# Kernel tuning notes

Measured on AMD Instinct MI355X. Metric: run time of the kernel, lower is better.

Reference implementation:

```python
import jax, jax.numpy as jnp
import numpy as np

B, S, D = 2, 2048, 2048
VOCAB = 32000
CUTOFFS = [1000, 2000, 5000, VOCAB]  # torch appends vocab_size
N_CLUSTERS = 3
HEAD_SIZE = CUTOFFS[0] + N_CLUSTERS  # 1003
LN_EPS = 1e-5
INIT = 0.02


def setup_inputs() -> dict:
    key = jax.random.key(0)
    ks = jax.random.split(key, 10)
    inp = {
        "x": jax.random.normal(ks[0], (B, S, D), dtype=jnp.float32),
        "targets": jax.random.randint(ks[1], (B, S), 0, VOCAB, dtype=jnp.int32),
        "gamma": jnp.ones((D,), jnp.float32),
        "beta": jnp.zeros((D,), jnp.float32),
        "head_w": jax.random.normal(ks[2], (HEAD_SIZE, D), jnp.float32) * INIT,
    }
    # tail clusters: hsz = D // 4**i, osz = cutoffs[i] - cutoffs[i-1]
    for i in range(1, 4):
        hsz = D // (4 ** i)
        osz = CUTOFFS[i] - CUTOFFS[i - 1]
        inp[f"t{i}_w1"] = jax.random.normal(ks[2 + 2 * i], (hsz, D), jnp.float32) * INIT
        inp[f"t{i}_w2"] = jax.random.normal(ks[3 + 2 * i], (osz, hsz), jnp.float32) * INIT
    return inp


def reference(x, targets, gamma, beta, head_w, t1_w1, t1_w2, t2_w1, t2_w2, t3_w1, t3_w2):
    # LayerNorm over last dim
    mu = jnp.mean(x, axis=-1, keepdims=True)
    var = jnp.mean(jnp.square(x - mu), axis=-1, keepdims=True)
    xn = (x - mu) * jax.lax.rsqrt(var + LN_EPS) * gamma + beta

    # shift: predict token t+1 from hidden t
    h = xn[:, :-1, :].reshape(-1, x.shape[-1])      # [N, D]
    lbl = targets[:, 1:].reshape(-1)                # [N]
    n = h.shape[0]
    rows = jnp.arange(n)

    # head: shortlist (first cutoff) + one logit per tail cluster
    head_lp = jax.nn.log_softmax(h @ head_w.T, axis=-1)  # [N, 1003]
    out = head_lp[rows, jnp.clip(lbl, 0, CUTOFFS[0] - 1)]

    tails = [(t1_w1, t1_w2), (t2_w1, t2_w2), (t3_w1, t3_w2)]
    for i, (w1, w2) in enumerate(tails):
        low, high = CUTOFFS[i], CUTOFFS[i + 1]
        tail_lp = jax.nn.log_softmax((h @ w1.T) @ w2.T, axis=-1)  # [N, osz]
        rel = jnp.clip(lbl - low, 0, high - low - 1)
        lp = head_lp[:, CUTOFFS[0] + i] + tail_lp[rows, rel]
        out = jnp.where((lbl >= low) & (lbl < high), lp, out)

    return -jnp.mean(out)  # NLL loss, matches .loss of AdaptiveLogSoftmaxWithLoss
```

## Files before the change

kernel.cpp:

```cpp
#include <hip/hip_runtime.h>
#include <hip/hip_bf16.h>
#include <math.h>

#define BB 2
#define SS 2048
#define DD 2048
#define NR (BB*(SS-1))
#define NRP 4096
#define MT_LD 768
#define MT_P2 512
#define MT_P3 640

#define L2E 1.4426950408889634f
#define LN2F 0.6931471805599453f
#define LSE_SHIFT 4.0f
#define LSE_NC (-LSE_SHIFT * L2E)
#define WSCALE 16.0f
#define WINV   0.0625f

typedef short  bh8   __attribute__((ext_vector_type(8)));
typedef float  f32x4 __attribute__((ext_vector_type(4)));
typedef long   l64x2 __attribute__((ext_vector_type(2)));

__device__ inline float bfl(unsigned short b) { return __uint_as_float(((unsigned)b) << 16); }
__device__ inline float expsh(float v) { return __builtin_amdgcn_exp2f(fmaf(v, L2E, LSE_NC)); }

__device__ inline float block_sum256(float v) {
    __shared__ float tmp[4];
    #pragma unroll
    for (int o = 32; o > 0; o >>= 1) v += __shfl_down(v, o, 64);
    int lane = threadIdx.x & 63, w = threadIdx.x >> 6;
    if (lane == 0) tmp[w] = v;
    __syncthreads();
    float r = tmp[0] + tmp[1] + tmp[2] + tmp[3];
    __syncthreads();
    return r;
}

__device__ inline unsigned pack_fp8x4(float a, float b, float c, float d) {
    unsigned r = 0;
    r = __builtin_amdgcn_cvt_pk_fp8_f32(a, b, r, false);
    r = __builtin_amdgcn_cvt_pk_fp8_f32(c, d, r, true);
    return r;
}

struct CastSegs {
    const float* src[7];
    void* dst[7];
    int n_src[7];
    int n_tot[7];
    int b0[7];
    int isfp8[7];
    float scl[7];
};
struct AParams {
    const float* x; const float* gamma; const float* beta;
    unsigned char* h8;
    CastSegs sg; int castBlocks;
    const int* targets;
    int *relH, *rel1, *rel2, *rel3;
    float *S0, *S1, *S2, *out;
};

__global__ __launch_bounds__(256) void stageA(AParams p) {
    int blk = blockIdx.x, tid = threadIdx.x;
    if (blk < NRP) {
        int n = blk;
        unsigned char* hr = p.h8 + (size_t)n * DD;
        if (n >= NR) { *(uint2*)(hr + tid * 8) = make_uint2(0,0); return; }
        int b = n / (SS - 1), t = n % (SS - 1);
        const float4* xr = (const float4*)(p.x + (size_t)(b * SS + t) * DD);
        float4 a = xr[tid * 2];
        float4 c = xr[tid * 2 + 1];
        float sum = a.x + a.y + a.z + a.w + c.x + c.y + c.z + c.w;
        sum = block_sum256(sum);
        float mu = sum * (1.0f / DD);
        float d[8] = {a.x-mu, a.y-mu, a.z-mu, a.w-mu, c.x-mu, c.y-mu, c.z-mu, c.w-mu};
        float sq = 0.f;
        #pragma unroll
        for (int i = 0; i < 8; ++i) sq += d[i] * d[i];
        sq = block_sum256(sq);
        float rstd = rsqrtf(sq * (1.0f / DD) + 1e-5f);
        const float4* g4 = (const float4*)p.gamma;
        const float4* be4 = (const float4*)p.beta;
        float4 g1 = g4[tid*2], g2 = g4[tid*2+1];
        float4 b1 = be4[tid*2], b2 = be4[tid*2+1];
        float gg[8] = {g1.x,g1.y,g1.z,g1.w,g2.x,g2.y,g2.z,g2.w};
        float bb[8] = {b1.x,b1.y,b1.z,b1.w,b2.x,b2.y,b2.z,b2.w};
        float o[8];
        #pragma unroll
        for (int i = 0; i < 8; ++i) o[i] = d[i] * rstd * gg[i] + bb[i];
        uint2 pk;
        pk.x = pack_fp8x4(o[0], o[1], o[2], o[3]);
        pk.y = pack_fp8x4(o[4], o[5], o[6], o[7]);
        *(uint2*)(hr + tid * 8) = pk;
        return;
    }
    blk -= NRP;
    if (blk < p.castBlocks) {
        int k = 0;
        #pragma unroll
        for (int i = 1; i < 7; ++i) if (blk >= p.sg.b0[i]) k = i;
        int i4 = (blk - p.sg.b0[k]) * 1024 + tid * 4;
        if (i4 >= p.sg.n_tot[k]) return;
        float4 v = make_float4(0.f,0.f,0.f,0.f);
        if (i4 < p.sg.n_src[k]) v = *(const float4*)(p.sg.src[k] + i4);
        if (p.sg.isfp8[k]) {
            unsigned pk = pack_fp8x4(v.x * WSCALE, v.y * WSCALE, v.z * WSCALE, v.w * WSCALE);
            *(unsigned*)((unsigned char*)p.sg.dst[k] + i4) = pk;
        } else {
            float sc = p.sg.scl[k];
            __align__(8) __hip_bfloat16 o[4] = {
                __float2bfloat16(v.x * sc), __float2bfloat16(v.y * sc),
                __float2bfloat16(v.z * sc), __float2bfloat16(v.w * sc)};
            *(uint2*)((__hip_bfloat16*)p.sg.dst[k] + i4) = *(uint2*)o;
        }
        return;
    }
    blk -= p.castBlocks;
    int n = blk * 256 + tid;
    if (n >= NRP) return;
    int lbl = -1;
    if (n < NR) {
        int b = n / (SS - 1), t = n % (SS - 1);
        lbl = p.targets[b * SS + t + 1];
    }
    bool v = n < NR;
    p.relH[n] = v ? (lbl < 1000 ? lbl : 999) : -1;
    int r1 = lbl - 1000;  p.rel1[n] = v ? (r1 < 0 ? 0 : (r1 > 999   ? 999   : r1)) : -1;
    int r2 = lbl - 2000;  p.rel2[n] = v ? (r2 < 0 ? 0 : (r2 > 2999  ? 2999  : r2)) : -1;
    int r3 = lbl - 5000;  p.rel3[n] = v ? (r3 < 0 ? 0 : (r3 > 26999 ? 26999 : r3)) : -1;
    p.S0[n] = 0.f; p.S1[n] = 0.f; p.S2[n] = 0.f;
    if (n == 0) p.out[0] = 0.f;
}

__global__ __launch_bounds__(256) void megaF(
        const unsigned char* __restrict__ A,
        const unsigned char* __restrict__ W,
        __hip_bfloat16* __restrict__ megaT,
        const int* __restrict__ relH,
        float* __restrict__ S0, float* __restrict__ aux) {
    __shared__ __align__(16) unsigned char smF[2][12288];
    int tid = threadIdx.x, wv = tid >> 6, lane = tid & 63;
    int row0 = blockIdx.y * 64, col0 = blockIdx.x * 128;
    int wrow = (wv >> 1) * 32, wcol = (wv & 1) * 64;
    f32x4 acc[2][4];
    #pragma unroll
    for (int i = 0; i < 2; ++i)
        #pragma unroll
        for (int j = 0; j < 4; ++j) acc[i][j] = (f32x4){0.f,0.f,0.f,0.f};
    int sr = lane >> 2;
    int kp = (((lane & 3) ^ (sr & 3)) * 16);
    int mrow = lane & 15;
    int qx = (((lane >> 4) ^ (lane & 3)) * 16);

    auto stage = [&](int buf, int k0) {
        {
            int r = wv * 16 + sr;
            const void* ga = A + (size_t)(row0 + r) * DD + k0 + kp;
            void* la = (char*)&smF[buf][0] + wv * 1024 + lane * 16;
            __builtin_amdgcn_global_load_lds(
                (const __attribute__((address_space(1))) void*)ga,
                (__attribute__((address_space(3))) void*)la, 16, 0, 0);
        }
        #pragma unroll
        for (int i = 0; i < 2; ++i) {
            int chunk = wv * 2 + i;
            int r = chunk * 16 + sr;
            const void* gw = W + (size_t)(col0 + r) * DD + k0 + kp;
            void* lw = (char*)&smF[buf][4096] + chunk * 1024 + lane * 16;
            __builtin_amdgcn_global_load_lds(
                (const __attribute__((address_space(1))) void*)gw,
                (__attribute__((address_space(3))) void*)lw, 16, 0, 0);
        }
    };

    stage(0, 0);
    asm volatile("s_waitcnt vmcnt(0)" ::: "memory");
    __builtin_amdgcn_s_barrier();
    __builtin_amdgcn_sched_barrier(0);
    int cur = 0;
    for (int k0 = 0; k0 < DD; k0 += 64) {
        if (k0 + 64 < DD) stage(cur ^ 1, k0 + 64);
        const unsigned char* As = &smF[cur][0];
        const unsigned char* Ws = &smF[cur][4096];
        l64x2 af[2], bfr[4];
        #pragma unroll
        for (int t = 0; t < 2; ++t)
            af[t]  = *(const l64x2*)(As + (wrow + t*16 + mrow) * 64 + qx);
        #pragma unroll
        for (int t = 0; t < 4; ++t)
            bfr[t] = *(const l64x2*)(Ws + (wcol + t*16 + mrow) * 64 + qx);
        #pragma unroll
        for (int s = 0; s < 2; ++s)
            #pragma unroll
            for (int i = 0; i < 2; ++i)
                #pragma unroll
                for (int j = 0; j < 4; ++j)
                    acc[i][j] = __builtin_amdgcn_mfma_f32_16x16x32_fp8_fp8(
                        af[i][s], bfr[j][s], acc[i][j], 0, 0, 0);
        asm volatile("s_waitcnt vmcnt(0) lgkmcnt(0)" ::: "memory");
        __builtin_amdgcn_s_barrier();
        __builtin_amdgcn_sched_barrier(0);
        cur ^= 1;
    }
    int ccol = lane & 15, g = lane >> 4;
    if (blockIdx.x < 8) {
        int grs[2][4], rh[2][4];
        float ps[2][4];
        #pragma unroll
        for (int i = 0; i < 2; ++i)
            #pragma unroll
            for (int r = 0; r < 4; ++r) {
                grs[i][r] = row0 + wrow + i*16 + g*4 + r;
                rh[i][r] = relH[grs[i][r]];
                ps[i][r] = 0.f;
            }
        #pragma unroll
        for (int i = 0; i < 2; ++i)
            #pragma unroll
            for (int j = 0; j < 4; ++j) {
                int gc = col0 + wcol + j*16 + ccol;
                bool inr = gc < 1003;
                #pragma unroll
                for (int r = 0; r < 4; ++r) {
                    float v = acc[i][j][r] * WINV;
                    if (gc == rh[i][r]) aux[grs[i][r]*8 + 0] = v;
                    if (gc >= 1000 && gc < 1003) aux[grs[i][r]*8 + 2 + (gc - 1000)] = v;
                    ps[i][r] += inr ? expsh(v) : 0.f;
                }
            }
        #pragma unroll
        for (int off = 1; off < 16; off <<= 1)
            #pragma unroll
            for (int i = 0; i < 2; ++i)
                #pragma unroll
                for (int r = 0; r < 4; ++r) ps[i][r] += __shfl_xor(ps[i][r], off, 64);
        if (ccol == 0)
            #pragma unroll
            for (int i = 0; i < 2; ++i)
                #pragma unroll
                for (int r = 0; r < 4; ++r) atomicAdd(&S0[grs[i][r]], ps[i][r]);
    } else {
        int cb = col0 - 1024 + wcol;
        #pragma unroll
        for (int i = 0; i < 2; ++i) {
            size_t gr0 = row0 + wrow + i*16 + g*4;
            #pragma unroll
            for (int j = 0; j < 4; ++j) {
                size_t gc = cb + j*16 + ccol;
                #pragma unroll
                for (int r = 0; r < 4; ++r)
                    megaT[(gr0 + r) * MT_LD + gc] = __float2bfloat16(acc[i][j][r] * WINV);
            }
        }
    }
}

__device__ void tail_gemm(const __hip_bfloat16* A, int lda,
        const __hip_bfloat16* W, int K, int bx, int by, int validCols,
        const int* rel, float* S, float* tgt, char* sm) {
    __hip_bfloat16* As = (__hip_bfloat16*)sm;
    __hip_bfloat16* Ws = (__hip_bfloat16*)(sm + 4096);
    int tid = threadIdx.x, wv = tid >> 6, lane = tid & 63;
    int row0 = by * 64, col0 = bx * 128;
    int wrow = (wv >> 1) * 32, wcol = (wv & 1) * 64;
    f32x4 acc[2][4];
    #pragma unroll
    for (int i = 0; i < 2; ++i)
        #pragma unroll
        for (int j = 0; j < 4; ++j) acc[i][j] = (f32x4){0.f,0.f,0.f,0.f};
    int sr = lane >> 2;
    int sk = (((lane & 3) ^ (sr & 3)) * 8);
    int mrow = lane & 15;
    int qx = (((lane >> 4) ^ (lane & 3)) * 16);

    for (int k0 = 0; k0 < K; k0 += 32) {
        __syncthreads();
        #pragma unroll
        for (int i = 0; i < 3; ++i) {
            int c = wv * 3 + i;
            const __hip_bfloat16* gsrc;
            char* ldst;
            if (c < 4) {
                gsrc = A + (size_t)(row0 + c * 16 + sr) * lda + k0 + sk;
                ldst = (char*)As + c * 1024 + lane * 16;
            } else {
                int cw = c - 4;
                gsrc = W + (size_t)(col0 + cw * 16 + sr) * K + k0 + sk;
                ldst = (char*)Ws + cw * 1024 + lane * 16;
            }
            __builtin_amdgcn_global_load_lds(
                (const __attribute__((address_space(1))) void*)gsrc,
                (__attribute__((address_space(3))) void*)ldst, 16, 0, 0);
        }
        __syncthreads();
        bh8 af[2], bfr[4];
        #pragma unroll
        for (int t = 0; t < 2; ++t)
            af[t] = *(const bh8*)((const char*)As + (wrow + t*16 + mrow) * 64 + qx);
        #pragma unroll
        for (int t = 0; t < 4; ++t)
            bfr[t] = *(const bh8*)((const char*)Ws + (wcol + t*16 + mrow) * 64 + qx);
        #pragma unroll
        for (int i = 0; i < 2; ++i)
            #pragma unroll
            for (int j = 0; j < 4; ++j)
                acc[i][j] = __builtin_amdgcn_mfma_f32_16x16x32_bf16(af[i], bfr[j], acc[i][j], 0, 0, 0);
    }
    int ccol = lane & 15, g = lane >> 4;
    int grs[2][4], rh[2][4];
    float p[2][4];
    #pragma unroll
    for (int i = 0; i < 2; ++i)
        #pragma unroll
        for (int r = 0; r < 4; ++r) {
            grs[i][r] = row0 + wrow + i*16 + g*4 + r;
            rh[i][r] = rel[grs[i][r]];
            p[i][r] = 0.f;
        }
    #pragma unroll
    for (int i = 0; i < 2; ++i)
        #pragma unroll
        for (int j = 0; j < 4; ++j) {
            int gc = col0 + wcol + j*16 + ccol;
            bool inr = gc < validCols;
            #pragma unroll
            for (int r = 0; r < 4; ++r) {
                float v = acc[i][j][r];
                if (gc == rh[i][r]) tgt[grs[i][r]] = v;
                p[i][r] += inr ? expsh(v) : 0.f;
            }
        }
    #pragma unroll
    for (int off = 1; off < 16; off <<= 1)
        #pragma unroll
        for (int i = 0; i < 2; ++i)
            #pragma unroll
            for (int r = 0; r < 4; ++r) p[i][r] += __shfl_xor(p[i][r], off, 64);
    if (ccol == 0)
        #pragma unroll
        for (int i = 0; i < 2; ++i)
            #pragma unroll
            for (int r = 0; r < 4; ++r) atomicAdd(&S[grs[i][r]], p[i][r]);
}

#define T3_TILES 1688
#define T3_SPLIT 32
#define T3_TPC   53
__device__ void t3_partial_body(const __hip_bfloat16* megaT,
        const __hip_bfloat16* w2b, float* pS, int idx, int tid, float* red ) {
    int rg = idx >> 5, cs = idx & 31;
    int wv = tid >> 6, lane = tid & 63;
    int q = lane >> 4, cm = lane & 15;
    int row0 = rg * 64;
    bh8 af[4];
    #pragma unroll
    for (int h = 0; h < 4; ++h)
        af[h] = *(const bh8*)(megaT + (size_t)(row0 + h*16 + cm) * MT_LD + MT_P3 + q * 8);
    int tile0 = cs * T3_TPC;
    int tile1 = tile0 + T3_TPC; if (tile1 > T3_TILES) tile1 = T3_TILES;
    float s[4][4];
    #pragma unroll
    for (int h = 0; h < 4; ++h)
        #pragma unroll
        for (int r = 0; r < 4; ++r) s[h][r] = 0.f;
    int ot = tile0 + wv;
    auto baddr = [&](int t) {
        int tc = t < tile1 ? t : tile1 - 1;
        return (const bh8*)(w2b + (size_t)(tc * 16 + cm) * 32 + q * 8);
    };
    bh8 p0 = *baddr(ot), p1 = *baddr(ot + 4), p2 = *baddr(ot + 8), p3 = *baddr(ot + 12);
    for (; ot < tile1; ot += 4) {
        bh8 bcur = p0;
        p0 = p1; p1 = p2; p2 = p3;
        int otn = ot + 16;
        if (otn < tile1)
            p3 = *(const bh8*)(w2b + (size_t)(otn * 16 + cm) * 32 + q * 8);
        f32x4 c[4];
        #pragma unroll
        for (int h = 0; h < 4; ++h)
            c[h] = __builtin_amdgcn_mfma_f32_16x16x32_bf16(af[h], bcur, (f32x4){0,0,0,0}, 0, 0, 0);
        #pragma unroll
        for (int h = 0; h < 4; ++h)
            #pragma unroll
            for (int r = 0; r < 4; ++r) s[h][r] += __builtin_amdgcn_exp2f(c[h][r]);
    }
    #pragma unroll
    for (int off = 1; off < 16; off <<= 1)
        #pragma unroll
        for (int h = 0; h < 4; ++h)
            #pragma unroll
            for (int r = 0; r < 4; ++r) s[h][r] += __shfl_xor(s[h][r], off, 64);
    if (cm == 0)
        #pragma unroll
        for (int h = 0; h < 4; ++h)
            #pragma unroll
            for (int r = 0; r < 4; ++r)
                red[wv * 64 + h*16 + q*4 + r] = s[h][r];
    __syncthreads();
    if (tid < 64)
        pS[(size_t)(row0 + tid) * T3_SPLIT + cs] =
            red[tid] + red[64 + tid] + red[128 + tid] + red[192 + tid];
}

__device__ void t3_gather_body(const __hip_bfloat16* megaT, const __hip_bfloat16* w2b,
        const int* rel3, float* tt2, int idx, int tid) {
    int n = idx * 256 + tid;
    if (n >= NR) return;
    int rc = rel3[n];
    const unsigned short* pa = (const unsigned short*)(megaT + (size_t)n * MT_LD + MT_P3);
    const unsigned short* pw = (const unsigned short*)(w2b + (size_t)rc * 32);
    float acc = 0.f;
    #pragma unroll
    for (int k = 0; k < 32; ++k) acc += bfl(pa[k]) * bfl(pw[k]);
    tt2[n] = acc;
}

#define NT3 (64 * T3_SPLIT)
#define NT1 512
#define NT2 1536
__global__ __launch_bounds__(256) void fatC(const __hip_bfloat16* __restrict__ megaT,
        const __hip_bfloat16* __restrict__ t1w2b, const __hip_bfloat16* __restrict__ t2w2b,
        const __hip_bfloat16* __restrict__ w2b3,
        const int* __restrict__ rel1, const int* __restrict__ rel2, const int* __restrict__ rel3,
        float* __restrict__ S1, float* __restrict__ S2, float* __restrict__ pS3,
        float* __restrict__ tt0, float* __restrict__ tt1, float* __restrict__ tt2) {
    __shared__ __align__(16) char sm[12288];
    int idx = blockIdx.x, tid = threadIdx.x;
    if (idx < NT3) { t3_partial_body(megaT, w2b3, pS3, idx, tid, (float*)sm); return; }
    idx -= NT3;
    if (idx < NT1) { tail_gemm(megaT, MT_LD, t1w2b, 512, idx % 8, idx / 8, 1000, rel1, S1, tt0, sm); return; }
    idx -= NT1;
    if (idx < NT2) { tail_gemm(megaT + MT_P2, MT_LD, t2w2b, 128, idx % 24, idx / 24, 3000, rel2, S2, tt1, sm); return; }
    idx -= NT2;
    t3_gather_body(megaT, w2b3, rel3, tt2, idx, tid);
}

__global__ __launch_bounds__(256) void final_kernel(const float* __restrict__ aux,
        const int* __restrict__ targets,
        const float* __restrict__ S0, const float* __restrict__ S1, const float* __restrict__ S2,
        const float* __restrict__ pS3,
        const float* __restrict__ tt0, const float* __restrict__ tt1, const float* __restrict__ tt2,
        float* __restrict__ out) {
    int n = blockIdx.x * 256 + threadIdx.x;
    float local = 0.f;
    if (n < NR) {
        int b = n / (SS - 1), t = n % (SS - 1);
        int lbl = targets[b * SS + t + 1];
        float lse = logf(S0[n]) + LSE_SHIFT;
        float o;
        if (lbl < 1000)      o = aux[n*8 + 0] - lse;
        else if (lbl < 2000) o = (aux[n*8 + 2] - lse) + (tt0[n] - (logf(S1[n]) + LSE_SHIFT));
        else if (lbl < 5000) o = (aux[n*8 + 3] - lse) + (tt1[n] - (logf(S2[n]) + LSE_SHIFT));
        else {
            float S3 = 0.f;
            const float4* p4 = (const float4*)(pS3 + (size_t)n * T3_SPLIT);
            #pragma unroll
            for (int c = 0; c < T3_SPLIT/4; ++c) {
                float4 v = p4[c];
                S3 += v.x + v.y + v.z + v.w;
            }
            S3 -= 8.0f;
            o = (aux[n*8 + 4] - lse) + (tt2[n] * LN2F - logf(S3));
        }
        local = o;
    }
    local = block_sum256(local);
    if (threadIdx.x == 0) atomicAdd(out, -local / (float)NR);
}

extern "C" void kernel_launch(void* const* d_in, const int* in_sizes, int n_in,
                              void* d_out, int out_size, void* d_ws, size_t ws_size,
                              hipStream_t stream) {
    const float* x      = (const float*)d_in[0];
    const int*   targets= (const int*)d_in[1];
    const float* gamma  = (const float*)d_in[2];
    const float* beta   = (const float*)d_in[3];
    const float* head_w = (const float*)d_in[4];
    const float* t1_w1  = (const float*)d_in[5];
    const float* t1_w2  = (const float*)d_in[6];
    const float* t2_w1  = (const float*)d_in[7];
    const float* t2_w2  = (const float*)d_in[8];
    const float* t3_w1  = (const float*)d_in[9];
    const float* t3_w2  = (const float*)d_in[10];
    (void)in_sizes; (void)n_in; (void)out_size; (void)ws_size;

    char* base = (char*)d_ws;
    size_t off = 0;
    auto ab = [&](size_t nbytes) { char* p = base + off; off += (nbytes + 15) & ~(size_t)15; return p; };
    unsigned char* h8     = (unsigned char*)ab((size_t)NRP * DD);
    unsigned char* w1cat8 = (unsigned char*)ab((size_t)1792 * DD);
    __hip_bfloat16* megaT = (__hip_bfloat16*)ab((size_t)NRP * MT_LD * 2);
    __hip_bfloat16* t1w2b = (__hip_bfloat16*)ab((size_t)1024 * 512 * 2);
    __hip_bfloat16* t2w2b = (__hip_bfloat16*)ab((size_t)3072 * 128 * 2);
    __hip_bfloat16* w2b3  = (__hip_bfloat16*)ab((size_t)27008 * 32 * 2);
    float* aux = (float*)ab((size_t)NRP * 8 * 4);
    float* pS3 = (float*)ab((size_t)NRP * T3_SPLIT * 4);
    float* S0  = (float*)ab(NRP * 4);
    float* S1  = (float*)ab(NRP * 4);
    float* S2  = (float*)ab(NRP * 4);
    int* relH  = (int*)ab(NRP * 4);
    int* rel1  = (int*)ab(NRP * 4);
    int* rel2  = (int*)ab(NRP * 4);
    int* rel3  = (int*)ab(NRP * 4);
    float* tt0 = (float*)ab(NRP * 4);
    float* tt1 = (float*)ab(NRP * 4);
    float* tt2 = (float*)ab(NRP * 4);

    AParams p;
    p.x = x; p.gamma = gamma; p.beta = beta; p.h8 = h8;
    p.targets = targets;
    p.relH = relH; p.rel1 = rel1; p.rel2 = rel2; p.rel3 = rel3;
    p.S0 = S0; p.S1 = S1; p.S2 = S2; p.out = (float*)d_out;
    const float* srcs[7] = {head_w, t1_w1, t2_w1, t3_w1, t1_w2, t2_w2, t3_w2};
    void* dsts[7] = {w1cat8, w1cat8 + (size_t)1024*2048, w1cat8 + (size_t)1536*2048,
                     w1cat8 + (size_t)1664*2048, t1w2b, t2w2b, w2b3};
    int nsrc[7] = {1003*2048, 512*2048, 128*2048, 32*2048, 1000*512, 3000*128, 27000*32};
    int ntot[7] = {1024*2048, 512*2048, 128*2048, 128*2048, 1024*512, 3072*128, 27008*32};
    int isf8[7] = {1, 1, 1, 1, 0, 0, 0};
    float scls[7] = {1.f, 1.f, 1.f, 1.f, 1.0f, 1.0f, L2E};
    int blk = 0;
    for (int i = 0; i < 7; ++i) {
        p.sg.src[i] = srcs[i]; p.sg.dst[i] = dsts[i];
        p.sg.n_src[i] = nsrc[i]; p.sg.n_tot[i] = ntot[i];
        p.sg.isfp8[i] = isf8[i];
        p.sg.scl[i] = scls[i];
        p.sg.b0[i] = blk;
        blk += (ntot[i] + 1023) / 1024;
    }
    p.castBlocks = blk;

    stageA<<<NRP + blk + 16, 256, 0, stream>>>(p);
    megaF<<<dim3(14, 64), 256, 0, stream>>>(h8, w1cat8, megaT, relH, S0, aux);
    fatC<<<NT3 + NT1 + NT2 + 16, 256, 0, stream>>>(megaT, t1w2b, t2w2b, w2b3,
            rel1, rel2, rel3, S1, S2, pS3, tt0, tt1, tt2);
    final_kernel<<<16, 256, 0, stream>>>(aux, targets, S0, S1, S2, pS3, tt0, tt1, tt2, (float*)d_out);
}
```

Measured before the change: 187.2 us.

## Compact rows per tail cluster and run tail GEMMs only on routed rows

Stage A now buckets each row by its target's cluster with atomic counters, writing a compacted row list, per-row compact index and relative label per tail. The tail GEMMs and the tail-3 partial softmax gather only those rows and exit early for tiles beyond each cluster's count. This removes the dense computation of every tail's logits for all rows, since the loss only needs each row's own cluster. It adds atomics, indirect row loads, an extra memset, and halves the tail-3 column split to make up for fewer row groups.

```diff
diff --git a/kernel.cpp b/kernel.cpp
--- a/kernel.cpp
+++ b/kernel.cpp
@@ -58,8 +58,12 @@
     unsigned char* h8;
     CastSegs sg; int castBlocks;
     const int* targets;
-    int *relH, *rel1, *rel2, *rel3;
-    float *S0, *S1, *S2, *out;
+    int *relH;
+    int *cnt;
+    int *rlist1, *rlist2, *rlist3;
+    int *cidx1, *cidx2, *cidx3;
+    int *rel1c, *rel2c, *rel3c;
+    float *S0, *S1c, *S2c, *out;
 };
 
 __global__ __launch_bounds__(256) void stageA(AParams p) {
@@ -127,10 +131,22 @@
     }
     bool v = n < NR;
     p.relH[n] = v ? (lbl < 1000 ? lbl : 999) : -1;
-    int r1 = lbl - 1000;  p.rel1[n] = v ? (r1 < 0 ? 0 : (r1 > 999   ? 999   : r1)) : -1;
-    int r2 = lbl - 2000;  p.rel2[n] = v ? (r2 < 0 ? 0 : (r2 > 2999  ? 2999  : r2)) : -1;
-    int r3 = lbl - 5000;  p.rel3[n] = v ? (r3 < 0 ? 0 : (r3 > 26999 ? 26999 : r3)) : -1;
-    p.S0[n] = 0.f; p.S1[n] = 0.f; p.S2[n] = 0.f;
+    if (v) {
+        if (lbl >= 1000 && lbl < 2000) {
+            int ci = atomicAdd(&p.cnt[0], 1);
+            p.rlist1[ci] = n; p.cidx1[n] = ci;
+            int r1 = lbl - 1000; p.rel1c[ci] = r1 > 999 ? 999 : r1;
+        } else if (lbl >= 2000 && lbl < 5000) {
+            int ci = atomicAdd(&p.cnt[1], 1);
+            p.rlist2[ci] = n; p.cidx2[n] = ci;
+            int r2 = lbl - 2000; p.rel2c[ci] = r2 > 2999 ? 2999 : r2;
+        } else if (lbl >= 5000) {
+            int ci = atomicAdd(&p.cnt[2], 1);
+            p.rlist3[ci] = n; p.cidx3[n] = ci;
+            int r3 = lbl - 5000; p.rel3c[ci] = r3 > 26999 ? 26999 : r3;
+        }
+    }
+    p.S0[n] = 0.f; p.S1c[n] = 0.f; p.S2c[n] = 0.f;
     if (n == 0) p.out[0] = 0.f;
 }
 
@@ -259,7 +275,8 @@
 
 __device__ void tail_gemm(const __hip_bfloat16* A, int lda,
         const __hip_bfloat16* W, int K, int bx, int by, int validCols,
-        const int* rel, float* S, float* tgt, char* sm) {
+        const int* relc, float* S, float* tgt, char* sm,
+        const int* rlist, int nrows) {
     __hip_bfloat16* As = (__hip_bfloat16*)sm;
     __hip_bfloat16* Ws = (__hip_bfloat16*)(sm + 4096);
     int tid = threadIdx.x, wv = tid >> 6, lane = tid & 63;
@@ -275,6 +292,17 @@
     int mrow = lane & 15;
     int qx = (((lane >> 4) ^ (lane & 3)) * 16);
 
+    const __hip_bfloat16* gA[3];
+    #pragma unroll
+    for (int i = 0; i < 3; ++i) {
+        int c = wv * 3 + i;
+        if (c < 4) {
+            int r = row0 + c * 16 + sr;
+            int orow = rlist[r < nrows ? r : nrows - 1];
+            gA[i] = A + (size_t)orow * lda + sk;
+        } else gA[i] = nullptr;
+    }
+
     for (int k0 = 0; k0 < K; k0 += 32) {
         __syncthreads();
         #pragma unroll
@@ -283,7 +311,7 @@
             const __hip_bfloat16* gsrc;
             char* ldst;
             if (c < 4) {
-                gsrc = A + (size_t)(row0 + c * 16 + sr) * lda + k0 + sk;
+                gsrc = gA[i] + k0;
                 ldst = (char*)As + c * 1024 + lane * 16;
             } else {
                 int cw = c - 4;
@@ -316,7 +344,7 @@
         #pragma unroll
         for (int r = 0; r < 4; ++r) {
             grs[i][r] = row0 + wrow + i*16 + g*4 + r;
-            rh[i][r] = rel[grs[i][r]];
+            rh[i][r] = relc[grs[i][r] < nrows ? grs[i][r] : 0];
             p[i][r] = 0.f;
         }
     #pragma unroll
@@ -328,7 +356,7 @@
             #pragma unroll
             for (int r = 0; r < 4; ++r) {
                 float v = acc[i][j][r];
-                if (gc == rh[i][r]) tgt[grs[i][r]] = v;
+                if (gc == rh[i][r] && grs[i][r] < nrows) tgt[grs[i][r]] = v;
                 p[i][r] += inr ? expsh(v) : 0.f;
             }
         }
@@ -342,22 +370,27 @@
         #pragma unroll
         for (int i = 0; i < 2; ++i)
             #pragma unroll
-            for (int r = 0; r < 4; ++r) atomicAdd(&S[grs[i][r]], p[i][r]);
+            for (int r = 0; r < 4; ++r)
+                if (grs[i][r] < nrows) atomicAdd(&S[grs[i][r]], p[i][r]);
 }
 
 #define T3_TILES 1688
-#define T3_SPLIT 32
-#define T3_TPC   53
+#define T3_SPLIT 16
+#define T3_TPC   106
 __device__ void t3_partial_body(const __hip_bfloat16* megaT,
-        const __hip_bfloat16* w2b, float* pS, int idx, int tid, float* red ) {
-    int rg = idx >> 5, cs = idx & 31;
+        const __hip_bfloat16* w2b, float* pS, const int* rlist3, int n3,
+        int idx, int tid, float* red ) {
+    int rg = idx >> 4, cs = idx & 15;
     int wv = tid >> 6, lane = tid & 63;
     int q = lane >> 4, cm = lane & 15;
     int row0 = rg * 64;
     bh8 af[4];
     #pragma unroll
-    for (int h = 0; h < 4; ++h)
-        af[h] = *(const bh8*)(megaT + (size_t)(row0 + h*16 + cm) * MT_LD + MT_P3 + q * 8);
+    for (int h = 0; h < 4; ++h) {
+        int r = row0 + h*16 + cm;
+        int orow = rlist3[r < n3 ? r : n3 - 1];
+        af[h] = *(const bh8*)(megaT + (size_t)orow * MT_LD + MT_P3 + q * 8);
+    }
     int tile0 = cs * T3_TPC;
     int tile1 = tile0 + T3_TPC; if (tile1 > T3_TILES) tile1 = T3_TILES;
     float s[4][4];
@@ -405,43 +438,65 @@
 }
 
 __device__ void t3_gather_body(const __hip_bfloat16* megaT, const __hip_bfloat16* w2b,
-        const int* rel3, float* tt2, int idx, int tid) {
-    int n = idx * 256 + tid;
-    if (n >= NR) return;
-    int rc = rel3[n];
-    const unsigned short* pa = (const unsigned short*)(megaT + (size_t)n * MT_LD + MT_P3);
+        const int* rlist3, const int* rel3c, int n3, float* tt2c, int idx, int tid) {
+    int ci = idx * 256 + tid;
+    if (ci >= n3) return;
+    int orow = rlist3[ci];
+    int rc = rel3c[ci];
+    const unsigned short* pa = (const unsigned short*)(megaT + (size_t)orow * MT_LD + MT_P3);
     const unsigned short* pw = (const unsigned short*)(w2b + (size_t)rc * 32);
     float acc = 0.f;
     #pragma unroll
     for (int k = 0; k < 32; ++k) acc += bfl(pa[k]) * bfl(pw[k]);
-    tt2[n] = acc;
+    tt2c[ci] = acc;
 }
 
 #define NT3 (64 * T3_SPLIT)
 #define NT1 512
 #define NT2 1536
+#define NGATH 16
 __global__ __launch_bounds__(256) void fatC(const __hip_bfloat16* __restrict__ megaT,
         const __hip_bfloat16* __restrict__ t1w2b, const __hip_bfloat16* __restrict__ t2w2b,
         const __hip_bfloat16* __restrict__ w2b3,
-        const int* __restrict__ rel1, const int* __restrict__ rel2, const int* __restrict__ rel3,
-        float* __restrict__ S1, float* __restrict__ S2, float* __restrict__ pS3,
-        float* __restrict__ tt0, float* __restrict__ tt1, float* __restrict__ tt2) {
+        const int* __restrict__ cnt,
+        const int* __restrict__ rlist1, const int* __restrict__ rlist2, const int* __restrict__ rlist3,
+        const int* __restrict__ rel1c, const int* __restrict__ rel2c, const int* __restrict__ rel3c,
+        float* __restrict__ S1c, float* __restrict__ S2c, float* __restrict__ pS3,
+        float* __restrict__ tt0c, float* __restrict__ tt1c, float* __restrict__ tt2c) {
     __shared__ __align__(16) char sm[12288];
     int idx = blockIdx.x, tid = threadIdx.x;
-    if (idx < NT3) { t3_partial_body(megaT, w2b3, pS3, idx, tid, (float*)sm); return; }
+    if (idx < NT3) {
+        int n3 = cnt[2];
+        if ((idx >> 4) * 64 >= n3) return;
+        t3_partial_body(megaT, w2b3, pS3, rlist3, n3, idx, tid, (float*)sm);
+        return;
+    }
     idx -= NT3;
-    if (idx < NT1) { tail_gemm(megaT, MT_LD, t1w2b, 512, idx % 8, idx / 8, 1000, rel1, S1, tt0, sm); return; }
+    if (idx < NT1) {
+        int n1 = cnt[0];
+        int by = idx / 8, bx = idx % 8;
+        if (by * 64 >= n1) return;
+        tail_gemm(megaT, MT_LD, t1w2b, 512, bx, by, 1000, rel1c, S1c, tt0c, sm, rlist1, n1);
+        return;
+    }
     idx -= NT1;
-    if (idx < NT2) { tail_gemm(megaT + MT_P2, MT_LD, t2w2b, 128, idx % 24, idx / 24, 3000, rel2, S2, tt1, sm); return; }
+    if (idx < NT2) {
+        int n2 = cnt[1];
+        int by = idx / 24, bx = idx % 24;
+        if (by * 64 >= n2) return;
+        tail_gemm(megaT + MT_P2, MT_LD, t2w2b, 128, bx, by, 3000, rel2c, S2c, tt1c, sm, rlist2, n2);
+        return;
+    }
     idx -= NT2;
-    t3_gather_body(megaT, w2b3, rel3, tt2, idx, tid);
+    t3_gather_body(megaT, w2b3, rlist3, rel3c, cnt[2], tt2c, idx, tid);
 }
 
 __global__ __launch_bounds__(256) void final_kernel(const float* __restrict__ aux,
         const int* __restrict__ targets,
-        const float* __restrict__ S0, const float* __restrict__ S1, const float* __restrict__ S2,
+        const float* __restrict__ S0, const float* __restrict__ S1c, const float* __restrict__ S2c,
         const float* __restrict__ pS3,
-        const float* __restrict__ tt0, const float* __restrict__ tt1, const float* __restrict__ tt2,
+        const float* __restrict__ tt0c, const float* __restrict__ tt1c, const float* __restrict__ tt2c,
+        const int* __restrict__ cidx1, const int* __restrict__ cidx2, const int* __restrict__ cidx3,
         float* __restrict__ out) {
     int n = blockIdx.x * 256 + threadIdx.x;
     float local = 0.f;
@@ -451,18 +506,23 @@
         float lse = logf(S0[n]) + LSE_SHIFT;
         float o;
         if (lbl < 1000)      o = aux[n*8 + 0] - lse;
-        else if (lbl < 2000) o = (aux[n*8 + 2] - lse) + (tt0[n] - (logf(S1[n]) + LSE_SHIFT));
-        else if (lbl < 5000) o = (aux[n*8 + 3] - lse) + (tt1[n] - (logf(S2[n]) + LSE_SHIFT));
-        else {
+        else if (lbl < 2000) {
+            int ci = cidx1[n];
+            o = (aux[n*8 + 2] - lse) + (tt0c[ci] - (logf(S1c[ci]) + LSE_SHIFT));
+        } else if (lbl < 5000) {
+            int ci = cidx2[n];
+            o = (aux[n*8 + 3] - lse) + (tt1c[ci] - (logf(S2c[ci]) + LSE_SHIFT));
+        } else {
+            int ci = cidx3[n];
             float S3 = 0.f;
-            const float4* p4 = (const float4*)(pS3 + (size_t)n * T3_SPLIT);
+            const float4* p4 = (const float4*)(pS3 + (size_t)ci * T3_SPLIT);
             #pragma unroll
             for (int c = 0; c < T3_SPLIT/4; ++c) {
                 float4 v = p4[c];
                 S3 += v.x + v.y + v.z + v.w;
             }
             S3 -= 8.0f;
-            o = (aux[n*8 + 4] - lse) + (tt2[n] * LN2F - logf(S3));
+            o = (aux[n*8 + 4] - lse) + (tt2c[ci] * LN2F - logf(S3));
         }
         local = o;
     }
@@ -498,21 +558,34 @@
     float* aux = (float*)ab((size_t)NRP * 8 * 4);
     float* pS3 = (float*)ab((size_t)NRP * T3_SPLIT * 4);
     float* S0  = (float*)ab(NRP * 4);
-    float* S1  = (float*)ab(NRP * 4);
-    float* S2  = (float*)ab(NRP * 4);
+    float* S1c = (float*)ab(NRP * 4);
+    float* S2c = (float*)ab(NRP * 4);
     int* relH  = (int*)ab(NRP * 4);
-    int* rel1  = (int*)ab(NRP * 4);
-    int* rel2  = (int*)ab(NRP * 4);
-    int* rel3  = (int*)ab(NRP * 4);
-    float* tt0 = (float*)ab(NRP * 4);
-    float* tt1 = (float*)ab(NRP * 4);
-    float* tt2 = (float*)ab(NRP * 4);
+    int* cnt   = (int*)ab(4 * 4);
+    int* rlist1= (int*)ab(NRP * 4);
+    int* rlist2= (int*)ab(NRP * 4);
+    int* rlist3= (int*)ab(NRP * 4);
+    int* cidx1 = (int*)ab(NRP * 4);
+    int* cidx2 = (int*)ab(NRP * 4);
+    int* cidx3 = (int*)ab(NRP * 4);
+    int* rel1c = (int*)ab(NRP * 4);
+    int* rel2c = (int*)ab(NRP * 4);
+    int* rel3c = (int*)ab(NRP * 4);
+    float* tt0c= (float*)ab(NRP * 4);
+    float* tt1c= (float*)ab(NRP * 4);
+    float* tt2c= (float*)ab(NRP * 4);
+
+    hipMemsetAsync(cnt, 0, 4 * 4, stream);
 
     AParams p;
     p.x = x; p.gamma = gamma; p.beta = beta; p.h8 = h8;
     p.targets = targets;
-    p.relH = relH; p.rel1 = rel1; p.rel2 = rel2; p.rel3 = rel3;
-    p.S0 = S0; p.S1 = S1; p.S2 = S2; p.out = (float*)d_out;
+    p.relH = relH;
+    p.cnt = cnt;
+    p.rlist1 = rlist1; p.rlist2 = rlist2; p.rlist3 = rlist3;
+    p.cidx1 = cidx1; p.cidx2 = cidx2; p.cidx3 = cidx3;
+    p.rel1c = rel1c; p.rel2c = rel2c; p.rel3c = rel3c;
+    p.S0 = S0; p.S1c = S1c; p.S2c = S2c; p.out = (float*)d_out;
     const float* srcs[7] = {head_w, t1_w1, t2_w1, t3_w1, t1_w2, t2_w2, t3_w2};
     void* dsts[7] = {w1cat8, w1cat8 + (size_t)1024*2048, w1cat8 + (size_t)1536*2048,
                      w1cat8 + (size_t)1664*2048, t1w2b, t2w2b, w2b3};
@@ -533,7 +606,9 @@
 
     stageA<<<NRP + blk + 16, 256, 0, stream>>>(p);
     megaF<<<dim3(14, 64), 256, 0, stream>>>(h8, w1cat8, megaT, relH, S0, aux);
-    fatC<<<NT3 + NT1 + NT2 + 16, 256, 0, stream>>>(megaT, t1w2b, t2w2b, w2b3,
-            rel1, rel2, rel3, S1, S2, pS3, tt0, tt1, tt2);
-    final_kernel<<<16, 256, 0, stream>>>(aux, targets, S0, S1, S2, pS3, tt0, tt1, tt2, (float*)d_out);
-}
+    fatC<<<NT3 + NT1 + NT2 + NGATH, 256, 0, stream>>>(megaT, t1w2b, t2w2b, w2b3,
+            cnt, rlist1, rlist2, rlist3, rel1c, rel2c, rel3c,
+            S1c, S2c, pS3, tt0c, tt1c, tt2c);
+    final_kernel<<<16, 256, 0, stream>>>(aux, targets, S0, S1c, S2c, pS3,
+            tt0c, tt1c, tt2c, cidx1, cidx2, cidx3, (float*)d_out);
+}
```

Result: faster. 176.1 us (-5.9%).
